# Kernel tuning notes

Hardware: AMD Instinct MI355X
Metric: run time of the kernel (lower is better)

Reference implementation:

```python
import jax, jax.numpy as jnp
import numpy as np
import math

N, C_S, C_Z, C_IPA, H, NQ, NV = 768, 384, 128, 16, 12, 4, 8


def setup_inputs() -> dict:
    key = jax.random.key(0)
    ks = jax.random.split(key, 16)
    inp = {
        "s": jax.random.normal(ks[0], (N, C_S), jnp.float32),
        "z": jax.random.normal(ks[1], (N, N, C_Z), jnp.float32),
        "rots": jax.random.normal(ks[2], (N, 3, 3), jnp.float32),
        "trans": jax.random.normal(ks[3], (N, 3), jnp.float32),
        "mask": jnp.ones((N,), jnp.float32),
    }
    sc = 0.02
    inp["Wq"] = jax.random.normal(ks[4], (C_S, H * C_IPA), jnp.float32) * sc
    inp["bq"] = jnp.zeros((H * C_IPA,), jnp.float32)
    inp["Wkv"] = jax.random.normal(ks[5], (C_S, H * 2 * C_IPA), jnp.float32) * sc
    inp["bkv"] = jnp.zeros((H * 2 * C_IPA,), jnp.float32)
    inp["Wq3"] = jax.random.normal(ks[6], (C_S, H * 3 * NQ), jnp.float32) * sc
    inp["bq3"] = jnp.zeros((H * 3 * NQ,), jnp.float32)
    inp["Wkv3"] = jax.random.normal(ks[7], (C_S, H * 3 * (NQ + NV)), jnp.float32) * sc
    inp["bkv3"] = jnp.zeros((H * 3 * (NQ + NV),), jnp.float32)
    inp["Wb"] = jax.random.normal(ks[8], (C_Z, H), jnp.float32) * sc
    inp["bb"] = jnp.zeros((H,), jnp.float32)
    inp["hw"] = jnp.zeros((H,), jnp.float32)
    inp["Wo"] = jax.random.normal(ks[9], (H * (C_Z + C_IPA + NV * 4), C_S), jnp.float32) * sc
    inp["bo"] = jnp.zeros((C_S,), jnp.float32)
    return inp


def reference(s, z, rots, trans, mask, Wq, bq, Wkv, bkv, Wq3, bq3, Wkv3, bkv3, Wb, bb, hw, Wo, bo):
    normsize = math.sqrt(1.0 / (3 * C_IPA))
    normsize_B = math.sqrt(1.0 / 3.0)
    normsize_hw = math.sqrt(1.0 / (3 * NQ * 9.0 / 2))

    # scalar Q/K/V: [N, H, C_IPA]
    Q = (s @ Wq + bq).reshape(N, H, C_IPA)
    KV = (s @ Wkv + bkv).reshape(N, H, 2, C_IPA)
    K, V = KV[..., 0, :], KV[..., 1, :]

    # query points: project, place into global frame via rigid transform
    Q3 = (s @ Wq3 + bq3).reshape(N, 3, NQ * H).swapaxes(-1, -2)        # [N, NQ*H, 3]
    Q3 = jnp.einsum('nij,nkj->nki', rots, Q3) + trans[:, None, :]
    Q3 = Q3.reshape(N, H, NQ, 3)

    KV3 = (s @ Wkv3 + bkv3).reshape(N, 3, H * (NQ + NV)).swapaxes(-1, -2)
    KV3 = jnp.einsum('nij,nkj->nki', rots, KV3) + trans[:, None, :]
    KV3 = KV3.reshape(N, H, NQ + NV, 3)
    K3, V3 = KV3[:, :, :NQ, :], KV3[:, :, NQ:, :]                      # points per head

    # pair bias [N, N, H]
    B = z @ Wb + bb

    # scalar attention logits + pair bias
    AT = jnp.einsum('ihc,jhc->ijh', Q, K) * normsize + B * normsize_B

    # point attention: squared distances [N, N, H, NQ]
    d2 = jnp.sum(jnp.square(Q3[:, None] - K3[None, :]), axis=-1)
    hw_sp = jax.nn.softplus(hw) * normsize_hw                          # [H]
    AT3 = -0.5 * jnp.sum(d2 * hw_sp[None, None, :, None], axis=-1)     # [N, N, H]

    # mask bias: large negative where either residue masked out
    mask2 = mask[:, None] * mask[None, :]
    B3 = (mask2 - 1.0) * 1e9                                           # [N, N]

    AT = jax.nn.softmax(AT + AT3 + B3[..., None], axis=-2)             # softmax over j

    # scalar value aggregation
    O = jnp.einsum('ijh,jhc->ihc', AT, V).reshape(N, -1)

    # point value aggregation, then map back to local frame (inverse transform)
    O3 = jnp.einsum('ijh,jhcd->ihcd', AT, V3).reshape(N, H * NV, 3)
    O3 = jnp.einsum('nji,nkj->nki', rots, O3 - trans[:, None, :])      # rots^T @ (O3 - t)
    O3_norm = jnp.sqrt(jnp.sum(jnp.square(O3), axis=-1) + 1e-20)       # [N, H*NV]

    # pair representation aggregation
    O_pair = jnp.einsum('ijh,ijc->ihc', AT, z).reshape(N, -1)

    O_final = jnp.concatenate((O, O3[..., 0], O3[..., 1], O3[..., 2], O3_norm, O_pair), axis=-1)
    return O_final @ Wo + bo
```

## Files before the change

kernel.cpp:

```cpp
#include <hip/hip_runtime.h>
#include <cstdint>


typedef __attribute__((ext_vector_type(8))) short short8;
typedef __attribute__((ext_vector_type(4))) short short4_t;
typedef __attribute__((ext_vector_type(4))) float f32x4;

__device__ __forceinline__ unsigned short f2bf(float f) {
    unsigned u = __float_as_uint(f);
    u = (u + 0x7FFFu + ((u >> 16) & 1u)) >> 16;
    return (unsigned short)u;
}
__device__ __forceinline__ float bf2f(unsigned short s) {
    return __uint_as_float(((unsigned)s) << 16);
}
__device__ __forceinline__ unsigned pk2(float lo, float hi) {
    return (unsigned)f2bf(lo) | ((unsigned)f2bf(hi) << 16);
}

__global__ __launch_bounds__(256) void proj_kernel(
    const float* __restrict__ s,
    const float* __restrict__ Wq,   const float* __restrict__ bq,
    const float* __restrict__ Wkv,  const float* __restrict__ bkv,
    const float* __restrict__ Wq3,  const float* __restrict__ bq3,
    const float* __restrict__ Wkv3, const float* __restrict__ bkv3,
    float* __restrict__ Qw, unsigned short* __restrict__ Kw,
    unsigned short* __restrict__ Vw,
    float* __restrict__ P3q, float* __restrict__ P3kv)
{
    __shared__ __align__(16) float s_lds[32 * 384];
    const int t  = threadIdx.x;
    const int r0 = blockIdx.x * 32;
    const int c0 = blockIdx.y * 128;

    for (int u = t; u < 3072; u += 256) {
        int r = u / 96, c4 = u - r * 96;
        *(float4*)&s_lds[r * 384 + c4 * 4] =
            *(const float4*)&s[(size_t)(r0 + r) * 384 + c4 * 4];
    }
    __syncthreads();

    const int rg = t >> 6;
    const int lc = t & 63;
    const int colA = c0 + lc;
    const int colB = c0 + lc + 64;

    const float *wpA, *wpB; int ldA, ldB; float biasA, biasB;
    {
        int col = colA;
        if (col < 192)      { wpA = Wq   + col;       ldA = 192; biasA = bq[col]; }
        else if (col < 576) { wpA = Wkv  + (col-192); ldA = 384; biasA = bkv[col-192]; }
        else if (col < 720) { wpA = Wq3  + (col-576); ldA = 144; biasA = bq3[col-576]; }
        else                { wpA = Wkv3 + (col-720); ldA = 432; biasA = bkv3[col-720]; }
        col = colB;
        if (col < 192)      { wpB = Wq   + col;       ldB = 192; biasB = bq[col]; }
        else if (col < 576) { wpB = Wkv  + (col-192); ldB = 384; biasB = bkv[col-192]; }
        else if (col < 720) { wpB = Wq3  + (col-576); ldB = 144; biasB = bq3[col-576]; }
        else                { wpB = Wkv3 + (col-720); ldB = 432; biasB = bkv3[col-720]; }
    }

    float acc0[8] = {}, acc1[8] = {};
    for (int k = 0; k < 384; k += 4) {
        float4 sv[8];
        #pragma unroll
        for (int r = 0; r < 8; r++)
            sv[r] = *(const float4*)&s_lds[(rg*8 + r) * 384 + k];
        #pragma unroll
        for (int kk = 0; kk < 4; kk++) {
            float w0 = wpA[(k + kk) * ldA];
            float w1 = wpB[(k + kk) * ldB];
            #pragma unroll
            for (int r = 0; r < 8; r++) {
                float sval = ((const float*)&sv[r])[kk];
                acc0[r] += sval * w0;
                acc1[r] += sval * w1;
            }
        }
    }

    #pragma unroll
    for (int q = 0; q < 2; q++) {
        int col   = q ? colB : colA;
        float bia = q ? biasB : biasA;
        #pragma unroll
        for (int r = 0; r < 8; r++) {
            int row = r0 + rg*8 + r;
            float v = (q ? acc1[r] : acc0[r]) + bia;
            if (col < 192) {
                Qw[(size_t)row*192 + col] = v;
            } else if (col < 576) {
                int c = col - 192, h = c >> 5, sub = c & 31;
                if (sub < 16) Kw[(size_t)row*192 + h*16 + sub]      = f2bf(v);
                else          Vw[(size_t)row*192 + h*16 + (sub-16)] = f2bf(v);
            } else if (col < 720) {
                P3q[(size_t)row*144 + (col-576)] = v;
            } else {
                P3kv[(size_t)row*432 + (col-720)] = v;
            }
        }
    }
}

__global__ __launch_bounds__(192) void rot3_kernel(
    const float* __restrict__ P3q, const float* __restrict__ P3kv,
    const float* __restrict__ rots, const float* __restrict__ trans,
    float* __restrict__ Q3w, unsigned short* __restrict__ K3w,
    unsigned short* __restrict__ V3w)
{
    const int n = blockIdx.x;
    const int t = threadIdx.x;
    float R[9];
    #pragma unroll
    for (int u = 0; u < 9; u++) R[u] = rots[n*9 + u];
    float T0 = trans[n*3+0], T1 = trans[n*3+1], T2 = trans[n*3+2];

    float p0, p1, p2;
    if (t < 48) {
        p0 = P3q[(size_t)n*144 + t];
        p1 = P3q[(size_t)n*144 + 48 + t];
        p2 = P3q[(size_t)n*144 + 96 + t];
    } else {
        int k = t - 48;
        p0 = P3kv[(size_t)n*432 + k];
        p1 = P3kv[(size_t)n*432 + 144 + k];
        p2 = P3kv[(size_t)n*432 + 288 + k];
    }
    float o0 = R[0]*p0 + R[1]*p1 + R[2]*p2 + T0;
    float o1 = R[3]*p0 + R[4]*p1 + R[5]*p2 + T1;
    float o2 = R[6]*p0 + R[7]*p1 + R[8]*p2 + T2;

    if (t < 48) {
        Q3w[(size_t)n*144 + t*3 + 0] = o0;
        Q3w[(size_t)n*144 + t*3 + 1] = o1;
        Q3w[(size_t)n*144 + t*3 + 2] = o2;
    } else {
        int k = t - 48, h = k / 12, m = k % 12;
        if (m < 4) {
            size_t base = (size_t)n*144 + (h*4 + m)*3;
            K3w[base+0] = f2bf(o0); K3w[base+1] = f2bf(o1); K3w[base+2] = f2bf(o2);
        } else {
            size_t base = (size_t)n*384 + (h*8 + (m-4))*4;
            V3w[base+0] = f2bf(o0); V3w[base+1] = f2bf(o1); V3w[base+2] = f2bf(o2);
        }
    }
}

__global__ __launch_bounds__(256, 3) void ipa_main(
    const float* __restrict__ z, const float* __restrict__ rots,
    const float* __restrict__ trans, const float* __restrict__ mask,
    const float* __restrict__ Wb, const float* __restrict__ bb,
    const float* __restrict__ hw,
    const float* __restrict__ Qw, const unsigned short* __restrict__ Kw,
    const unsigned short* __restrict__ Vw,
    const float* __restrict__ Q3w, const unsigned short* __restrict__ K3w,
    const unsigned short* __restrict__ V3w,
    unsigned short* __restrict__ OF)
{
    __shared__ __align__(16) unsigned short z_l[4096];
    __shared__ __align__(16) unsigned short wbT_l[16 * 136];
    __shared__ __align__(16) float          p_l[32 * 17];
    __shared__ __align__(16) unsigned short pT_l[16 * 40];
    __shared__ __align__(16) float          Q_lds[192];
    __shared__ __align__(16) float          Q3_lds[144];
    __shared__ float hw_lds[12], bb_lds[12], den_lds[12];

    const int i    = blockIdx.x;
    const int t    = threadIdx.x;
    const int lane = t & 63;
    const int wv   = t >> 6;
    const int g    = lane >> 4;
    const int lm   = lane & 15;

    if (t < 192) Q_lds[t]  = Qw[(size_t)i*192 + t];
    if (t < 144) Q3_lds[t] = Q3w[(size_t)i*144 + t];
    if (t < 12) {
        hw_lds[t] = log1pf(__expf(hw[t])) * 0.13608276348795434f;
        bb_lds[t] = bb[t];
    }
    if (t < 160) pT_l[480 + t] = 0;
    for (int u = t; u < 1536; u += 256) {
        int h = u % 12, c = u / 12;
        wbT_l[h*136 + c] = f2bf(Wb[c*12 + h]);
    }
    const float mask_i = mask[i];

    f32x4 opA = {0,0,0,0}, opB = {0,0,0,0};
    float oacc = 0.0f;
    float o3x = 0, o3y = 0, o3z = 0;
    float dena = 0;
    const int oh = t >> 4, oc = t & 15;
    int o3h = -1, o3v = 0;
    if (t >= 192)     { o3h = (t - 192) >> 3; o3v = (t - 192) & 7; }
    else if (t < 32)  { o3h = 8 + (t >> 3);   o3v = t & 7; }
    const int denh = (t >= 32 && t < 44) ? (t - 32) : -1;

    __syncthreads();

    for (int tile = 0; tile < 24; tile++) {
        const int j0 = tile * 32;

        {
            const int jj = t >> 3, c16 = t & 7;
            const float* zp = z + ((size_t)i*768 + j0 + jj)*128 + c16*16;
            float4 f0 = *(const float4*)(zp + 0);
            float4 f1 = *(const float4*)(zp + 4);
            float4 f2 = *(const float4*)(zp + 8);
            float4 f3 = *(const float4*)(zp + 12);
            int byteoff = ((jj >> 2)*8 + c16)*128 + (jj & 3)*32;
            uint4* dst = (uint4*)((char*)z_l + byteoff);
            dst[0] = uint4{pk2(f0.x,f0.y), pk2(f0.z,f0.w), pk2(f1.x,f1.y), pk2(f1.z,f1.w)};
            dst[1] = uint4{pk2(f2.x,f2.y), pk2(f2.z,f2.w), pk2(f3.x,f3.y), pk2(f3.z,f3.w)};
        }
        __syncthreads();

        if (wv == 0) {
            f32x4 ab0 = {0,0,0,0}, ab1 = {0,0,0,0};
            #pragma unroll
            for (int ks = 0; ks < 4; ks++) {
                short8 bf = *(const short8*)((const char*)wbT_l + lm*272 + ks*64 + g*16);
                int jj0 = lm;
                int ch0 = (jj0 >> 2)*8 + ks*2 + (g >> 1);
                short8 a0 = *(const short8*)((const char*)z_l + ch0*128 + (jj0 & 3)*32 + (g & 1)*16);
                ab0 = __builtin_amdgcn_mfma_f32_16x16x32_bf16(a0, bf, ab0, 0, 0, 0);
                int jj1 = 16 + lm;
                int ch1 = (jj1 >> 2)*8 + ks*2 + (g >> 1);
                short8 a1 = *(const short8*)((const char*)z_l + ch1*128 + (jj1 & 3)*32 + (g & 1)*16);
                ab1 = __builtin_amdgcn_mfma_f32_16x16x32_bf16(a1, bf, ab1, 0, 0, 0);
            }
            if (lm < 12) {
                #pragma unroll
                for (int r = 0; r < 4; r++) {
                    p_l[(g*4 + r)*17 + lm]        = ab0[r];
                    p_l[(16 + g*4 + r)*17 + lm]   = ab1[r];
                }
            }
        }
        __syncthreads();

        #pragma unroll
        for (int rep = 0; rep < 2; rep++) {
            int pr = t + rep*256;
            if (pr < 384) {
                int jj = pr / 12;
                int h  = pr - jj*12;
                int j  = j0 + jj;
                float Bv = p_l[jj*17 + h];
                const unsigned short* kp = Kw + (size_t)j*192 + h*16;
                short8 kA = *(const short8*)(kp);
                short8 kB = *(const short8*)(kp + 8);
                float qk = 0.0f;
                #pragma unroll
                for (int e = 0; e < 8; e++) qk += Q_lds[h*16 + e]     * bf2f((unsigned short)kA[e]);
                #pragma unroll
                for (int e = 0; e < 8; e++) qk += Q_lds[h*16 + 8 + e] * bf2f((unsigned short)kB[e]);
                const unsigned short* k3p = K3w + (size_t)j*144 + h*12;
                short4_t c0v = *(const short4_t*)(k3p);
                short4_t c1v = *(const short4_t*)(k3p + 4);
                short4_t c2v = *(const short4_t*)(k3p + 8);
                float d2 = 0.0f;
                #pragma unroll
                for (int e = 0; e < 4; e++) { float d = Q3_lds[h*12 + e]     - bf2f((unsigned short)c0v[e]); d2 += d*d; }
                #pragma unroll
                for (int e = 0; e < 4; e++) { float d = Q3_lds[h*12 + 4 + e] - bf2f((unsigned short)c1v[e]); d2 += d*d; }
                #pragma unroll
                for (int e = 0; e < 4; e++) { float d = Q3_lds[h*12 + 8 + e] - bf2f((unsigned short)c2v[e]); d2 += d*d; }
                float mj = mask[j];
                float lg = qk * 0.14433756729740643f
                         + (Bv + bb_lds[h]) * 0.5773502691896258f
                         - 0.5f * hw_lds[h] * d2
                         + (mask_i * mj - 1.0f) * 1e9f;
                float p = __expf(lg);
                p_l[jj*17 + h]  = p;
                pT_l[h*40 + jj] = f2bf(p);
            }
        }
        __syncthreads();

        {
            const int nt0 = wv*2;
            short8 ap = *(const short8*)((const char*)pT_l + lm*80 + g*16);
            short8 b0, b1;
            #pragma unroll
            for (int e = 0; e < 8; e++) {
                int jj  = g*8 + e;
                int sub = (jj >> 2)*8;
                int ro  = (jj & 3)*16;
                b0[e] = (short)z_l[(sub + nt0)     * 64 + ro + lm];
                b1[e] = (short)z_l[(sub + nt0 + 1) * 64 + ro + lm];
            }
            opA = __builtin_amdgcn_mfma_f32_16x16x32_bf16(ap, b0, opA, 0, 0, 0);
            opB = __builtin_amdgcn_mfma_f32_16x16x32_bf16(ap, b1, opB, 0, 0, 0);
        }
        if (t < 192) {
            #pragma unroll 8
            for (int jj = 0; jj < 32; jj++) {
                float p = p_l[jj*17 + oh];
                oacc += p * bf2f(Vw[(size_t)(j0 + jj)*192 + oh*16 + oc]);
            }
        }
        if (o3h >= 0) {
            #pragma unroll 8
            for (int jj = 0; jj < 32; jj++) {
                float p = p_l[jj*17 + o3h];
                short4_t v4 = *(const short4_t*)(V3w + (size_t)(j0 + jj)*384 + (o3h*8 + o3v)*4);
                o3x += p * bf2f((unsigned short)v4[0]);
                o3y += p * bf2f((unsigned short)v4[1]);
                o3z += p * bf2f((unsigned short)v4[2]);
            }
        }
        if (denh >= 0) {
            #pragma unroll 8
            for (int jj = 0; jj < 32; jj++) dena += p_l[jj*17 + denh];
        }
        __syncthreads();
    }

    if (denh >= 0) den_lds[denh] = dena;
    __syncthreads();

    const size_t ofb = (size_t)i * 2112;
    if (t < 192) {
        OF[ofb + t] = f2bf(oacc / den_lds[oh]);
    }
    if (o3h >= 0) {
        float den = den_lds[o3h];
        float m0 = o3x/den - trans[i*3+0];
        float m1 = o3y/den - trans[i*3+1];
        float m2 = o3z/den - trans[i*3+2];
        const float* R = rots + (size_t)i*9;
        float r0v = R[0]*m0 + R[3]*m1 + R[6]*m2;
        float r1v = R[1]*m0 + R[4]*m1 + R[7]*m2;
        float r2v = R[2]*m0 + R[5]*m1 + R[8]*m2;
        float nrm = sqrtf(r0v*r0v + r1v*r1v + r2v*r2v + 1e-20f);
        int hv = o3h*8 + o3v;
        OF[ofb + 192 + hv] = f2bf(r0v);
        OF[ofb + 288 + hv] = f2bf(r1v);
        OF[ofb + 384 + hv] = f2bf(r2v);
        OF[ofb + 480 + hv] = f2bf(nrm);
    }
    {
        const int nt0 = wv*2;
        #pragma unroll
        for (int r = 0; r < 4; r++) {
            int h = g*4 + r;
            if (h < 12) {
                float den = den_lds[h];
                OF[ofb + 576 + h*128 + nt0*16 + lm]     = f2bf(opA[r] / den);
                OF[ofb + 576 + h*128 + (nt0+1)*16 + lm] = f2bf(opB[r] / den);
            }
        }
    }
}

__global__ __launch_bounds__(256) void out_gemm(
    const unsigned short* __restrict__ OF, const float* __restrict__ Wo,
    float* __restrict__ part)
{
    __shared__ __align__(16) float aT[32 * 132];
    __shared__ __align__(16) float bt[32 * 68];
    const int t  = threadIdx.x;
    const int i0 = blockIdx.x * 128;
    const int c0 = blockIdx.y * 64;
    const int k0 = blockIdx.z * 352;
    const int r0 = (t & 15) * 8;
    const int c4 = (t >> 4) * 4;

    float acc[8][4] = {};

    for (int kt = 0; kt < 11; kt++) {
        const int kk0 = k0 + kt*32;
        __syncthreads();
        {
            int r = t >> 1, kh = (t & 1) * 16;
            const unsigned short* apg = OF + (size_t)(i0 + r)*2112 + kk0 + kh;
            short8 v0 = *(const short8*)apg;
            short8 v1 = *(const short8*)(apg + 8);
            #pragma unroll
            for (int e = 0; e < 8; e++) aT[(kh + e)*132 + r]     = bf2f((unsigned short)v0[e]);
            #pragma unroll
            for (int e = 0; e < 8; e++) aT[(kh + 8 + e)*132 + r] = bf2f((unsigned short)v1[e]);
        }
        {
            int k = t >> 3, c8 = (t & 7) * 8;
            const float* wpg = Wo + (size_t)(kk0 + k)*384 + c0 + c8;
            *(float4*)&bt[k*68 + c8]     = *(const float4*)wpg;
            *(float4*)&bt[k*68 + c8 + 4] = *(const float4*)(wpg + 4);
        }
        __syncthreads();
        #pragma unroll 4
        for (int kk = 0; kk < 32; kk++) {
            float4 a0 = *(float4*)&aT[kk*132 + r0];
            float4 a1 = *(float4*)&aT[kk*132 + r0 + 4];
            float4 bv = *(float4*)&bt[kk*68 + c4];
            #pragma unroll
            for (int ci = 0; ci < 4; ci++) {
                float b = ((const float*)&bv)[ci];
                acc[0][ci] += ((const float*)&a0)[0] * b;
                acc[1][ci] += ((const float*)&a0)[1] * b;
                acc[2][ci] += ((const float*)&a0)[2] * b;
                acc[3][ci] += ((const float*)&a0)[3] * b;
                acc[4][ci] += ((const float*)&a1)[0] * b;
                acc[5][ci] += ((const float*)&a1)[1] * b;
                acc[6][ci] += ((const float*)&a1)[2] * b;
                acc[7][ci] += ((const float*)&a1)[3] * b;
            }
        }
    }

    float* pb = part + (size_t)blockIdx.z * 294912;
    #pragma unroll
    for (int ri = 0; ri < 8; ri++) {
        float4 o = {acc[ri][0], acc[ri][1], acc[ri][2], acc[ri][3]};
        *(float4*)&pb[(size_t)(i0 + r0 + ri)*384 + c0 + c4] = o;
    }
}

__global__ __launch_bounds__(256) void reduce_out(
    const float* __restrict__ part, const float* __restrict__ bo,
    float* __restrict__ out)
{
    int idx = blockIdx.x * 256 + threadIdx.x;
    float v = bo[idx % 384];
    #pragma unroll
    for (int s = 0; s < 6; s++) v += part[(size_t)s * 294912 + idx];
    out[idx] = v;
}

extern "C" void kernel_launch(void* const* d_in, const int* in_sizes, int n_in,
                              void* d_out, int out_size, void* d_ws, size_t ws_size,
                              hipStream_t stream) {
    const float* s     = (const float*)d_in[0];
    const float* z     = (const float*)d_in[1];
    const float* rots  = (const float*)d_in[2];
    const float* trans = (const float*)d_in[3];
    const float* mask  = (const float*)d_in[4];
    const float* Wq    = (const float*)d_in[5];
    const float* bq    = (const float*)d_in[6];
    const float* Wkv   = (const float*)d_in[7];
    const float* bkv   = (const float*)d_in[8];
    const float* Wq3   = (const float*)d_in[9];
    const float* bq3   = (const float*)d_in[10];
    const float* Wkv3  = (const float*)d_in[11];
    const float* bkv3  = (const float*)d_in[12];
    const float* Wb    = (const float*)d_in[13];
    const float* bb    = (const float*)d_in[14];
    const float* hw    = (const float*)d_in[15];
    const float* Wo    = (const float*)d_in[16];
    const float* bo    = (const float*)d_in[17];
    float* out = (float*)d_out;

    char* ws = (char*)d_ws;
    float*          Qw   = (float*)(ws + 0);
    float*          Q3w  = (float*)(ws + 589824);
    unsigned short* Kw   = (unsigned short*)(ws + 1032192);
    unsigned short* Vw   = (unsigned short*)(ws + 1327104);
    unsigned short* K3w  = (unsigned short*)(ws + 1622016);
    unsigned short* V3w  = (unsigned short*)(ws + 1843200);
    float*          P3q  = (float*)(ws + 2433024);
    float*          P3kv = (float*)(ws + 2875392);
    unsigned short* OF   = (unsigned short*)(ws + 4202496);
    float*          part = (float*)(ws + 7446528);

    proj_kernel<<<dim3(24, 9), 256, 0, stream>>>(
        s, Wq, bq, Wkv, bkv, Wq3, bq3, Wkv3, bkv3, Qw, Kw, Vw, P3q, P3kv);
    rot3_kernel<<<768, 192, 0, stream>>>(P3q, P3kv, rots, trans, Q3w, K3w, V3w);
    ipa_main<<<768, 256, 0, stream>>>(
        z, rots, trans, mask, Wb, bb, hw, Qw, Kw, Vw, Q3w, K3w, V3w, OF);
    out_gemm<<<dim3(6, 6, 6), 256, 0, stream>>>(OF, Wo, part);
    reduce_out<<<1152, 256, 0, stream>>>(part, bo, out);
}
```

Measured before the change: 269.0 us.

## Split IPA key dimension across two blocks, prefetch z tiles, add combine kernel

Each query row is now handled by two blocks that each cover half of the key range. The blocks write unnormalized partial sums and denominators to a workspace, and a new combine kernel merges them, normalizes, and applies the inverse rigid transform. Inside the main kernel the next z tile is loaded into registers while the current one is processed, the LDS row stride is padded to reduce bank conflicts, and the bias MFMA is spread over two waves. Occupancy is raised to 6 blocks per SM to improve latency hiding. The cost is an extra kernel launch and extra partial-buffer traffic, and the softmax has no max subtraction, so summing the partial exps directly stays consistent with the original.

```diff
diff --git a/kernel.cpp b/kernel.cpp
--- a/kernel.cpp
+++ b/kernel.cpp
@@ -145,26 +145,26 @@
     }
 }
 
-__global__ __launch_bounds__(256, 3) void ipa_main(
-    const float* __restrict__ z, const float* __restrict__ rots,
-    const float* __restrict__ trans, const float* __restrict__ mask,
+__global__ __launch_bounds__(256, 6) void ipa_main(
+    const float* __restrict__ z, const float* __restrict__ mask,
     const float* __restrict__ Wb, const float* __restrict__ bb,
     const float* __restrict__ hw,
     const float* __restrict__ Qw, const unsigned short* __restrict__ Kw,
     const unsigned short* __restrict__ Vw,
     const float* __restrict__ Q3w, const unsigned short* __restrict__ K3w,
     const unsigned short* __restrict__ V3w,
-    unsigned short* __restrict__ OF)
-{
-    __shared__ __align__(16) unsigned short z_l[4096];
+    float* __restrict__ part3)
+{
+    __shared__ __align__(16) unsigned short z_l[64 * 88];
     __shared__ __align__(16) unsigned short wbT_l[16 * 136];
     __shared__ __align__(16) float          p_l[32 * 17];
     __shared__ __align__(16) unsigned short pT_l[16 * 40];
     __shared__ __align__(16) float          Q_lds[192];
     __shared__ __align__(16) float          Q3_lds[144];
-    __shared__ float hw_lds[12], bb_lds[12], den_lds[12];
-
-    const int i    = blockIdx.x;
+    __shared__ float hw_lds[12], bb_lds[12];
+
+    const int i     = blockIdx.x >> 1;
+    const int chunk = blockIdx.x & 1;
     const int t    = threadIdx.x;
     const int lane = t & 63;
     const int wv   = t >> 6;
@@ -194,45 +194,49 @@
     else if (t < 32)  { o3h = 8 + (t >> 3);   o3v = t & 7; }
     const int denh = (t >= 32 && t < 44) ? (t - 32) : -1;
 
+    const int jj  = t >> 3, c16 = t & 7;
+    const float* zbase = z + ((size_t)i*768 + chunk*384 + jj)*128 + c16*16;
+    const int sidx = ((jj >> 2)*8 + c16)*88 + (jj & 3)*16;
+    float4 pf0, pf1, pf2, pf3;
+    pf0 = *(const float4*)(zbase + 0);
+    pf1 = *(const float4*)(zbase + 4);
+    pf2 = *(const float4*)(zbase + 8);
+    pf3 = *(const float4*)(zbase + 12);
+
     __syncthreads();
 
-    for (int tile = 0; tile < 24; tile++) {
-        const int j0 = tile * 32;
+    for (int tile = 0; tile < 12; tile++) {
+        const int j0 = chunk*384 + tile*32;
 
         {
-            const int jj = t >> 3, c16 = t & 7;
-            const float* zp = z + ((size_t)i*768 + j0 + jj)*128 + c16*16;
-            float4 f0 = *(const float4*)(zp + 0);
-            float4 f1 = *(const float4*)(zp + 4);
-            float4 f2 = *(const float4*)(zp + 8);
-            float4 f3 = *(const float4*)(zp + 12);
-            int byteoff = ((jj >> 2)*8 + c16)*128 + (jj & 3)*32;
-            uint4* dst = (uint4*)((char*)z_l + byteoff);
-            dst[0] = uint4{pk2(f0.x,f0.y), pk2(f0.z,f0.w), pk2(f1.x,f1.y), pk2(f1.z,f1.w)};
-            dst[1] = uint4{pk2(f2.x,f2.y), pk2(f2.z,f2.w), pk2(f3.x,f3.y), pk2(f3.z,f3.w)};
-        }
-        __syncthreads();
-
-        if (wv == 0) {
-            f32x4 ab0 = {0,0,0,0}, ab1 = {0,0,0,0};
+            uint4* dst = (uint4*)&z_l[sidx];
+            dst[0] = uint4{pk2(pf0.x,pf0.y), pk2(pf0.z,pf0.w), pk2(pf1.x,pf1.y), pk2(pf1.z,pf1.w)};
+            dst[1] = uint4{pk2(pf2.x,pf2.y), pk2(pf2.z,pf2.w), pk2(pf3.x,pf3.y), pk2(pf3.z,pf3.w)};
+        }
+        if (tile + 1 < 12) {
+            const float* np = zbase + (size_t)(tile + 1) * 32 * 128;
+            pf0 = *(const float4*)(np + 0);
+            pf1 = *(const float4*)(np + 4);
+            pf2 = *(const float4*)(np + 8);
+            pf3 = *(const float4*)(np + 12);
+        }
+        __syncthreads();
+
+        if (wv < 2) {
+            f32x4 ab = {0,0,0,0};
+            const int jt = wv;
             #pragma unroll
             for (int ks = 0; ks < 4; ks++) {
-                short8 bf = *(const short8*)((const char*)wbT_l + lm*272 + ks*64 + g*16);
-                int jj0 = lm;
-                int ch0 = (jj0 >> 2)*8 + ks*2 + (g >> 1);
-                short8 a0 = *(const short8*)((const char*)z_l + ch0*128 + (jj0 & 3)*32 + (g & 1)*16);
-                ab0 = __builtin_amdgcn_mfma_f32_16x16x32_bf16(a0, bf, ab0, 0, 0, 0);
-                int jj1 = 16 + lm;
-                int ch1 = (jj1 >> 2)*8 + ks*2 + (g >> 1);
-                short8 a1 = *(const short8*)((const char*)z_l + ch1*128 + (jj1 & 3)*32 + (g & 1)*16);
-                ab1 = __builtin_amdgcn_mfma_f32_16x16x32_bf16(a1, bf, ab1, 0, 0, 0);
+                short8 bf = *(const short8*)&wbT_l[lm*136 + ks*32 + g*8];
+                int jr = jt*16 + lm;
+                int ch = (jr >> 2)*8 + ks*2 + (g >> 1);
+                short8 a = *(const short8*)&z_l[ch*88 + (jr & 3)*16 + (g & 1)*8];
+                ab = __builtin_amdgcn_mfma_f32_16x16x32_bf16(a, bf, ab, 0, 0, 0);
             }
             if (lm < 12) {
                 #pragma unroll
-                for (int r = 0; r < 4; r++) {
-                    p_l[(g*4 + r)*17 + lm]        = ab0[r];
-                    p_l[(16 + g*4 + r)*17 + lm]   = ab1[r];
-                }
+                for (int r = 0; r < 4; r++)
+                    p_l[(jt*16 + g*4 + r)*17 + lm] = ab[r];
             }
         }
         __syncthreads();
@@ -241,10 +245,10 @@
         for (int rep = 0; rep < 2; rep++) {
             int pr = t + rep*256;
             if (pr < 384) {
-                int jj = pr / 12;
-                int h  = pr - jj*12;
-                int j  = j0 + jj;
-                float Bv = p_l[jj*17 + h];
+                int jjq = pr / 12;
+                int h   = pr - jjq*12;
+                int j   = j0 + jjq;
+                float Bv = p_l[jjq*17 + h];
                 const unsigned short* kp = Kw + (size_t)j*192 + h*16;
                 short8 kA = *(const short8*)(kp);
                 short8 kB = *(const short8*)(kp + 8);
@@ -270,8 +274,8 @@
                          - 0.5f * hw_lds[h] * d2
                          + (mask_i * mj - 1.0f) * 1e9f;
                 float p = __expf(lg);
-                p_l[jj*17 + h]  = p;
-                pT_l[h*40 + jj] = f2bf(p);
+                p_l[jjq*17 + h]  = p;
+                pT_l[h*40 + jjq] = f2bf(p);
             }
         }
         __syncthreads();
@@ -282,27 +286,27 @@
             short8 b0, b1;
             #pragma unroll
             for (int e = 0; e < 8; e++) {
-                int jj  = g*8 + e;
-                int sub = (jj >> 2)*8;
-                int ro  = (jj & 3)*16;
-                b0[e] = (short)z_l[(sub + nt0)     * 64 + ro + lm];
-                b1[e] = (short)z_l[(sub + nt0 + 1) * 64 + ro + lm];
+                int jje = g*8 + e;
+                int su  = (jje >> 2)*8;
+                int ro  = (jje & 3)*16;
+                b0[e] = (short)z_l[(su + nt0)     * 88 + ro + lm];
+                b1[e] = (short)z_l[(su + nt0 + 1) * 88 + ro + lm];
             }
             opA = __builtin_amdgcn_mfma_f32_16x16x32_bf16(ap, b0, opA, 0, 0, 0);
             opB = __builtin_amdgcn_mfma_f32_16x16x32_bf16(ap, b1, opB, 0, 0, 0);
         }
         if (t < 192) {
             #pragma unroll 8
-            for (int jj = 0; jj < 32; jj++) {
-                float p = p_l[jj*17 + oh];
-                oacc += p * bf2f(Vw[(size_t)(j0 + jj)*192 + oh*16 + oc]);
+            for (int jjq = 0; jjq < 32; jjq++) {
+                float p = p_l[jjq*17 + oh];
+                oacc += p * bf2f(Vw[(size_t)(j0 + jjq)*192 + oh*16 + oc]);
             }
         }
         if (o3h >= 0) {
             #pragma unroll 8
-            for (int jj = 0; jj < 32; jj++) {
-                float p = p_l[jj*17 + o3h];
-                short4_t v4 = *(const short4_t*)(V3w + (size_t)(j0 + jj)*384 + (o3h*8 + o3v)*4);
+            for (int jjq = 0; jjq < 32; jjq++) {
+                float p = p_l[jjq*17 + o3h];
+                short4_t v4 = *(const short4_t*)(V3w + (size_t)(j0 + jjq)*384 + (o3h*8 + o3v)*4);
                 o3x += p * bf2f((unsigned short)v4[0]);
                 o3y += p * bf2f((unsigned short)v4[1]);
                 o3z += p * bf2f((unsigned short)v4[2]);
@@ -310,45 +314,65 @@
         }
         if (denh >= 0) {
             #pragma unroll 8
-            for (int jj = 0; jj < 32; jj++) dena += p_l[jj*17 + denh];
-        }
-        __syncthreads();
-    }
-
-    if (denh >= 0) den_lds[denh] = dena;
-    __syncthreads();
-
-    const size_t ofb = (size_t)i * 2112;
-    if (t < 192) {
-        OF[ofb + t] = f2bf(oacc / den_lds[oh]);
-    }
+            for (int jjq = 0; jjq < 32; jjq++) dena += p_l[jjq*17 + denh];
+        }
+        __syncthreads();
+    }
+
+    float* pb = part3 + (size_t)blockIdx.x * 2048;
+    if (t < 192) pb[t] = oacc;
     if (o3h >= 0) {
-        float den = den_lds[o3h];
-        float m0 = o3x/den - trans[i*3+0];
-        float m1 = o3y/den - trans[i*3+1];
-        float m2 = o3z/den - trans[i*3+2];
-        const float* R = rots + (size_t)i*9;
-        float r0v = R[0]*m0 + R[3]*m1 + R[6]*m2;
-        float r1v = R[1]*m0 + R[4]*m1 + R[7]*m2;
-        float r2v = R[2]*m0 + R[5]*m1 + R[8]*m2;
-        float nrm = sqrtf(r0v*r0v + r1v*r1v + r2v*r2v + 1e-20f);
-        int hv = o3h*8 + o3v;
-        OF[ofb + 192 + hv] = f2bf(r0v);
-        OF[ofb + 288 + hv] = f2bf(r1v);
-        OF[ofb + 384 + hv] = f2bf(r2v);
-        OF[ofb + 480 + hv] = f2bf(nrm);
-    }
+        int base = 192 + (o3h*8 + o3v)*3;
+        pb[base+0] = o3x; pb[base+1] = o3y; pb[base+2] = o3z;
+    }
+    if (denh >= 0) pb[2016 + denh] = dena;
     {
         const int nt0 = wv*2;
         #pragma unroll
         for (int r = 0; r < 4; r++) {
             int h = g*4 + r;
             if (h < 12) {
-                float den = den_lds[h];
-                OF[ofb + 576 + h*128 + nt0*16 + lm]     = f2bf(opA[r] / den);
-                OF[ofb + 576 + h*128 + (nt0+1)*16 + lm] = f2bf(opB[r] / den);
-            }
-        }
+                pb[480 + h*128 + nt0*16 + lm]       = opA[r];
+                pb[480 + h*128 + (nt0 + 1)*16 + lm] = opB[r];
+            }
+        }
+    }
+}
+
+__global__ __launch_bounds__(256) void combine_kernel(
+    const float* __restrict__ part3, const float* __restrict__ rots,
+    const float* __restrict__ trans, unsigned short* __restrict__ OF)
+{
+    const int i = blockIdx.x;
+    const int t = threadIdx.x;
+    const float* pa = part3 + (size_t)i*2*2048;
+    const float* pb = pa + 2048;
+    __shared__ float den_s[12];
+    if (t < 12) den_s[t] = pa[2016 + t] + pb[2016 + t];
+    __syncthreads();
+
+    const size_t ofb = (size_t)i * 2112;
+    if (t < 192) OF[ofb + t] = f2bf((pa[t] + pb[t]) / den_s[t >> 4]);
+    if (t < 96) {
+        int h = t >> 3, v = t & 7;
+        float den = den_s[h];
+        int base = 192 + t*3;
+        float m0 = (pa[base+0] + pb[base+0]) / den - trans[i*3+0];
+        float m1 = (pa[base+1] + pb[base+1]) / den - trans[i*3+1];
+        float m2 = (pa[base+2] + pb[base+2]) / den - trans[i*3+2];
+        const float* R = rots + (size_t)i*9;
+        float r0v = R[0]*m0 + R[3]*m1 + R[6]*m2;
+        float r1v = R[1]*m0 + R[4]*m1 + R[7]*m2;
+        float r2v = R[2]*m0 + R[5]*m1 + R[8]*m2;
+        float nrm = sqrtf(r0v*r0v + r1v*r1v + r2v*r2v + 1e-20f);
+        int hv = h*8 + v;
+        OF[ofb + 192 + hv] = f2bf(r0v);
+        OF[ofb + 288 + hv] = f2bf(r1v);
+        OF[ofb + 384 + hv] = f2bf(r2v);
+        OF[ofb + 480 + hv] = f2bf(nrm);
+    }
+    for (int u = t; u < 1536; u += 256) {
+        OF[ofb + 576 + u] = f2bf((pa[480 + u] + pb[480 + u]) / den_s[u >> 7]);
     }
 }
 
@@ -407,11 +431,11 @@
         }
     }
 
-    float* pb = part + (size_t)blockIdx.z * 294912;
+    float* pbv = part + (size_t)blockIdx.z * 294912;
     #pragma unroll
     for (int ri = 0; ri < 8; ri++) {
         float4 o = {acc[ri][0], acc[ri][1], acc[ri][2], acc[ri][3]};
-        *(float4*)&pb[(size_t)(i0 + r0 + ri)*384 + c0 + c4] = o;
+        *(float4*)&pbv[(size_t)(i0 + r0 + ri)*384 + c0 + c4] = o;
     }
 }
 
@@ -459,13 +483,15 @@
     float*          P3q  = (float*)(ws + 2433024);
     float*          P3kv = (float*)(ws + 2875392);
     unsigned short* OF   = (unsigned short*)(ws + 4202496);
-    float*          part = (float*)(ws + 7446528);
+    float*          part3 = (float*)(ws + 7446528);
+    float*          part  = (float*)(ws + 7446528);
 
     proj_kernel<<<dim3(24, 9), 256, 0, stream>>>(
         s, Wq, bq, Wkv, bkv, Wq3, bq3, Wkv3, bkv3, Qw, Kw, Vw, P3q, P3kv);
     rot3_kernel<<<768, 192, 0, stream>>>(P3q, P3kv, rots, trans, Q3w, K3w, V3w);
-    ipa_main<<<768, 256, 0, stream>>>(
-        z, rots, trans, mask, Wb, bb, hw, Qw, Kw, Vw, Q3w, K3w, V3w, OF);
+    ipa_main<<<1536, 256, 0, stream>>>(
+        z, mask, Wb, bb, hw, Qw, Kw, Vw, Q3w, K3w, V3w, part3);
+    combine_kernel<<<768, 256, 0, stream>>>(part3, rots, trans, OF);
     out_gemm<<<dim3(6, 6, 6), 256, 0, stream>>>(OF, Wo, part);
     reduce_out<<<1152, 256, 0, stream>>>(part, bo, out);
 }
```

After: 416.2 us. 54.7% more time.
